# Performance work log

Measured on AMD Instinct MI355X. Metric: run time of the kernel, lower is better.

## Reference

```python
import jax, jax.numpy as jnp
import numpy as np

B, C, H, W = 4, 512, 64, 64
CQ = C // 8


def setup_inputs() -> dict:
    key = jax.random.key(0)
    ks = jax.random.split(key, 8)
    s_in = 1.0 / np.sqrt(C)
    return {
        "x": jax.random.normal(ks[0], (B, C, H, W), jnp.float32),
        "wq": jax.random.normal(ks[1], (CQ, C), jnp.float32) * s_in,
        "bq": jax.random.normal(ks[2], (CQ,), jnp.float32) * 0.01,
        "wk": jax.random.normal(ks[3], (CQ, C), jnp.float32) * s_in,
        "bk": jax.random.normal(ks[4], (CQ,), jnp.float32) * 0.01,
        "wv": jax.random.normal(ks[5], (C, C), jnp.float32) * s_in,
        "bv": jax.random.normal(ks[6], (C,), jnp.float32) * 0.01,
        "gamma": jax.random.normal(ks[7], (1,), jnp.float32) * 0.1,
    }


def reference(x, wq, bq, wk, bk, wv, bv, gamma):
    b, c, h, w = x.shape
    n = h * w
    xf = x.reshape(b, c, n)  # [B, C, N]; 1x1 conv == channel matmul
    q = jnp.einsum("oc,bcn->bon", wq, xf) + bq[None, :, None]  # [B, CQ, N]
    k = jnp.einsum("oc,bcn->bon", wk, xf) + bk[None, :, None]  # [B, CQ, N]
    v = jnp.einsum("oc,bcn->bon", wv, xf) + bv[None, :, None]  # [B, C, N]
    energy = jnp.einsum("bcn,bcm->bnm", q, k)  # [B, N, N]
    attn = jax.nn.softmax(energy, axis=-1)
    out = jnp.einsum("bcm,bnm->bcn", v, attn)  # [B, C, N]
    out = out.reshape(b, c, h, w)
    return gamma[0] * out + x
```

## Files before the change

kernel.cpp:

```cpp
#include <hip/hip_runtime.h>
#include <hip/hip_bf16.h>

#define BATCH 4
#define CH    512
#define NPIX  4096
#define LOG2E 1.4426950408889634f

#define BOFF  327680
#define WTOT  328320
#define PSTR 264

typedef float v4f __attribute__((ext_vector_type(4)));
typedef short v8s __attribute__((ext_vector_type(8)));
typedef unsigned short u16;

__device__ __forceinline__ float b2f(u16 v){
    union { unsigned u; float f; } x; x.u = ((unsigned)v) << 16; return x.f;
}
__device__ __forceinline__ u16 f2b(float f){
    union { float f; unsigned u; } x; x.f = f;
    unsigned r = x.u + 0x7fffu + ((x.u >> 16) & 1u);
    return (u16)(r >> 16);
}
__device__ __forceinline__ void f2b2(float a, float b, u16* o){
    union { __hip_bfloat162 v; u16 s[2]; } u;
    u.v = __float22bfloat162_rn(make_float2(a, b));
    o[0] = u.s[0]; o[1] = u.s[1];
}
__device__ __forceinline__ v4f mfma16(v8s a, v8s b, v4f c){
    return __builtin_amdgcn_mfma_f32_16x16x32_bf16(a, b, c, 0, 0, 0);
}
__device__ __forceinline__ float load_s(const void* p, size_t idx, int isf32){
    return isf32 ? ((const float*)p)[idx] : b2f(((const u16*)p)[idx]);
}

__global__ void detect_kernel(const unsigned* __restrict__ x, int* __restrict__ flag){
    __shared__ int cnt;
    if (threadIdx.x == 0) cnt = 0;
    __syncthreads();
    int c = 0;
    for (int i = threadIdx.x; i < 1024; i += 64){
        unsigned e = (x[i] >> 23) & 0xFFu;
        if (e >= 64u && e < 192u) c++;
    }
    atomicAdd(&cnt, c);
    __syncthreads();
    if (threadIdx.x == 0) flag[0] = (cnt > 512) ? 1 : 0;
}

__global__ __launch_bounds__(256) void prep_kernel(
    const void* __restrict__ wq, const void* __restrict__ bq,
    const void* __restrict__ wk, const void* __restrict__ bk,
    const void* __restrict__ wv, const void* __restrict__ bv,
    u16* __restrict__ wall, const int* __restrict__ flag)
{
    const int isf32 = flag[0];
    int i = blockIdx.x * 256 + threadIdx.x;
    if (i >= WTOT) return;
    float v;
    if (i < BOFF){
        int o = i >> 9, c = i & 511;
        if (o < 64)       v = load_s(wq, (size_t)o * 512 + c, isf32);
        else if (o < 128) v = load_s(wk, (size_t)(o - 64) * 512 + c, isf32);
        else              v = load_s(wv, (size_t)(o - 128) * 512 + c, isf32);
    } else {
        int o = i - BOFF;
        if (o < 64)       v = load_s(bq, o, isf32);
        else if (o < 128) v = load_s(bk, o - 64, isf32);
        else              v = load_s(bv, o - 128, isf32);
    }
    wall[i] = f2b(v);
}

__global__ __launch_bounds__(512, 2) void proj_kernel(
    const void* __restrict__ x, const u16* __restrict__ wall,
    u16* __restrict__ Qf, u16* __restrict__ Kf, u16* __restrict__ Vf,
    u16* __restrict__ xbf, const int* __restrict__ flag)
{
    const int isf32 = flag[0];
    const int ntile = blockIdx.x, b = blockIdx.y;
    const int n0 = ntile * 64;
    const int t = threadIdx.x, lane = t & 63, w = t >> 6, q = lane >> 4, col = lane & 15;

    __shared__ __align__(16) u16 xT[2][64 * 40];

    const int rrow  = t >> 4;
    const int ncol4 = (t & 15) * 4;
    const size_t xbase = (size_t)b * CH * NPIX + n0 + ncol4;

    v4f acc[5][4];
    #pragma unroll
    for (int i = 0; i < 5; i++)
        #pragma unroll
        for (int j = 0; j < 4; j++) acc[i][j] = (v4f){0.f, 0.f, 0.f, 0.f};

    #define LOADX(dst_f4, cb_) do {                                          \
        const size_t src = xbase + (size_t)((cb_) * 32 + rrow) * NPIX;       \
        if (isf32) dst_f4 = *(const float4*)((const float*)x + src);         \
        else {                                                               \
            union { uint2 v; float2 f; } ldu;                                \
            ldu.v = *(const uint2*)((const u16*)x + src);                    \
            dst_f4.x = ldu.f.x; dst_f4.y = ldu.f.y; dst_f4.z = 0; dst_f4.w = 0; \
        }                                                                    \
    } while (0)

    #define CVT4(vals_, f4_) do {                                            \
        if (isf32){ f2b2(f4_.x, f4_.y, &vals_[0]); f2b2(f4_.z, f4_.w, &vals_[2]); } \
        else { union { float2 f; uint2 v; } uu; uu.f = make_float2(f4_.x, f4_.y);   \
               union { uint2 v; u16 s[4]; } ss; ss.v = uu.v;                 \
               vals_[0]=ss.s[0]; vals_[1]=ss.s[1]; vals_[2]=ss.s[2]; vals_[3]=ss.s[3]; } \
    } while (0)

    float4 g_next;
    {
        float4 g0; LOADX(g0, 0);
        u16 vals[4]; CVT4(vals, g0);
        #pragma unroll
        for (int i = 0; i < 4; i++) xT[0][(ncol4 + i) * 40 + rrow] = vals[i];
        *(uint2*)&xbf[(size_t)(b * CH + rrow) * NPIX + n0 + ncol4] = *(uint2*)vals;
        LOADX(g_next, 1);
    }
    __syncthreads();

    for (int cb = 0; cb < 16; cb++){
        const int buf = cb & 1;
        const int c0 = cb * 32 + q * 8;

        v8s wf[5];
        #pragma unroll
        for (int ct = 0; ct < 5; ct++)
            wf[ct] = *(const v8s*)&wall[(size_t)(80 * w + 16 * ct + col) * 512 + c0];

        v8s a[4];
        #pragma unroll
        for (int g = 0; g < 4; g++)
            a[g] = *(const v8s*)&xT[buf][(16 * g + col) * 40 + q * 8];

        if (cb < 15){
            u16 vals[4]; CVT4(vals, g_next);
            #pragma unroll
            for (int i = 0; i < 4; i++) xT[buf ^ 1][(ncol4 + i) * 40 + rrow] = vals[i];
            *(uint2*)&xbf[(size_t)(b * CH + (cb + 1) * 32 + rrow) * NPIX + n0 + ncol4] = *(uint2*)vals;
            if (cb < 14) LOADX(g_next, cb + 2);
        }

        #pragma unroll
        for (int ct = 0; ct < 5; ct++)
            #pragma unroll
            for (int g = 0; g < 4; g++)
                acc[ct][g] = mfma16(a[g], wf[ct], acc[ct][g]);
        __syncthreads();
    }
    #undef LOADX
    #undef CVT4

    const u16* ball = wall + BOFF;
    #pragma unroll
    for (int ct = 0; ct < 5; ct++){
        const int o = 80 * w + 16 * ct + col;
        const float bv_ = b2f(ball[o]);
        #pragma unroll
        for (int g = 0; g < 4; g++){
            const int nb = n0 + 16 * g + 4 * q;
            if (o < 64){
                const int k = o;
                size_t base = (size_t)b * NPIX * 64
                    + ((size_t)((nb >> 4) * 2 + (k >> 5))) * 512
                    + ((k & 31) >> 3) * 128 + (nb & 15) * 8 + (k & 7);
                #pragma unroll
                for (int r = 0; r < 4; r++)
                    Qf[base + r * 8] = f2b((acc[ct][g][r] + bv_) * LOG2E);
            } else if (o < 128){
                const int k = o - 64;
                size_t base = (size_t)b * NPIX * 64
                    + ((size_t)((nb >> 4) * 2 + (k >> 5))) * 512
                    + ((k & 31) >> 3) * 128 + (nb & 15) * 8 + (k & 7);
                #pragma unroll
                for (int r = 0; r < 4; r++)
                    Kf[base + r * 8] = f2b(acc[ct][g][r] + bv_);
            } else {
                const int c = o - 128;
                size_t base = (size_t)b * CH * NPIX
                    + ((size_t)((c >> 4) * 128 + (nb >> 5))) * 512
                    + ((nb & 31) >> 3) * 128 + (c & 15) * 8 + (nb & 7);
                union { uint2 u; u16 s[4]; } ov;
                #pragma unroll
                for (int r = 0; r < 4; r++)
                    ov.s[r] = f2b(acc[ct][g][r] + bv_);
                *(uint2*)&Vf[base] = ov.u;
            }
        }
    }
}

__global__ __launch_bounds__(512, 2) void attn_kernel(
    const u16* __restrict__ Qf, const u16* __restrict__ Kf, const u16* __restrict__ Vf,
    const u16* __restrict__ xbf, const void* __restrict__ gamma,
    void* __restrict__ out, const int* __restrict__ flag)
{
    const int isf32 = flag[0];
    const int bid = blockIdx.x;
    const int csplit = bid & 1;
    const int b      = (bid >> 1) & 3;
    const int ntile  = bid >> 3;
    const int n0 = ntile * 128;

    const int t = threadIdx.x, lane = t & 63, w = t >> 6, q = lane >> 4, col = lane & 15;
    const int nh = w & 1;
    const int ws = w >> 1;

    __shared__ __align__(16) u16  Plds[2][128 * PSTR];
    __shared__ __align__(16) float lsum[8][64];

    const u16* Qb = Qf + (size_t)b * NPIX * 64;
    const u16* Kb = Kf + (size_t)b * NPIX * 64;
    const u16* Vb = Vf + (size_t)b * CH * NPIX;

    v8s qa[4][2];
    #pragma unroll
    for (int g = 0; g < 4; g++)
        #pragma unroll
        for (int c2 = 0; c2 < 2; c2++)
            qa[g][c2] = *(const v8s*)&Qb[(size_t)((((n0 + 64 * nh) >> 4) + g) * 2 + c2) * 512 + lane * 8];

    float lreg[4][4];
    #pragma unroll
    for (int g = 0; g < 4; g++)
        #pragma unroll
        for (int r = 0; r < 4; r++) lreg[g][r] = 0.f;

    v4f oacc[4][4];
    #pragma unroll
    for (int i = 0; i < 4; i++)
        #pragma unroll
        for (int j = 0; j < 4; j++) oacc[i][j] = (v4f){0.f, 0.f, 0.f, 0.f};

    const int ms    = 64 * ws;
    const int cslab = csplit * 256 + 64 * ws;

    for (int it = 0; it < 16; it++){
        const int m0 = it * 256;
        const int buf = it & 1;

        v8s kf[4][2];
        #pragma unroll
        for (int mt = 0; mt < 4; mt++)
            #pragma unroll
            for (int c2 = 0; c2 < 2; c2++)
                kf[mt][c2] = *(const v8s*)&Kb[(size_t)((((m0 + ms) >> 4) + mt) * 2 + c2) * 512 + lane * 8];

        #pragma unroll
        for (int g = 0; g < 4; g++){
            #pragma unroll
            for (int mt = 0; mt < 4; mt++){
                v4f sv = (v4f){-64.f, -64.f, -64.f, -64.f};
                sv = mfma16(qa[g][0], kf[mt][0], sv);
                sv = mfma16(qa[g][1], kf[mt][1], sv);
                #pragma unroll
                for (int r = 0; r < 4; r++){
                    float p = exp2f(fminf(sv[r], 30.f));
                    lreg[g][r] += p;
                    Plds[buf][(64 * nh + 16 * g + 4 * q + r) * PSTR + ms + 16 * mt + col] = f2b(p);
                }
            }
        }

        __syncthreads();

        v8s va_c[4];
        #pragma unroll
        for (int ct = 0; ct < 4; ct++)
            va_c[ct] = *(const v8s*)&Vb[(size_t)(((cslab + 16 * ct) >> 4) * 128 + (m0 >> 5)) * 512 + lane * 8];
        #pragma unroll
        for (int kk = 0; kk < 8; kk++){
            v8s va_n[4];
            if (kk < 7){
                #pragma unroll
                for (int ct = 0; ct < 4; ct++)
                    va_n[ct] = *(const v8s*)&Vb[(size_t)(((cslab + 16 * ct) >> 4) * 128 + (m0 >> 5) + kk + 1) * 512 + lane * 8];
            }
            v8s pb[4];
            #pragma unroll
            for (int nt = 0; nt < 4; nt++)
                pb[nt] = *(const v8s*)&Plds[buf][(64 * nh + 16 * nt + col) * PSTR + 32 * kk + q * 8];
            #pragma unroll
            for (int ct = 0; ct < 4; ct++)
                #pragma unroll
                for (int nt = 0; nt < 4; nt++)
                    oacc[ct][nt] = mfma16(va_c[ct], pb[nt], oacc[ct][nt]);
            #pragma unroll
            for (int ct = 0; ct < 4; ct++) va_c[ct] = va_n[ct];
        }
    }

    #pragma unroll
    for (int mk = 1; mk < 16; mk <<= 1)
        #pragma unroll
        for (int g = 0; g < 4; g++)
            #pragma unroll
            for (int r = 0; r < 4; r++)
                lreg[g][r] += __shfl_xor(lreg[g][r], mk);
    if (col == 0){
        #pragma unroll
        for (int g = 0; g < 4; g++)
            #pragma unroll
            for (int r = 0; r < 4; r++)
                lsum[w][16 * g + 4 * q + r] = lreg[g][r];
    }
    __syncthreads();

    const float gam = load_s(gamma, 0, isf32);
    float linv[4];
    #pragma unroll
    for (int nt = 0; nt < 4; nt++){
        int nn = 16 * nt + col;
        float l = lsum[nh][nn] + lsum[2 + nh][nn] + lsum[4 + nh][nn] + lsum[6 + nh][nn];
        linv[nt] = gam / l;
    }

    const size_t boff = (size_t)b * CH * NPIX;
    #pragma unroll
    for (int ct = 0; ct < 4; ct++){
        #pragma unroll
        for (int rr = 0; rr < 4; rr++){
            int c = cslab + 16 * ct + 4 * q + rr;
            size_t base = boff + (size_t)c * NPIX + n0 + 64 * nh;
            #pragma unroll
            for (int nt = 0; nt < 4; nt++){
                int n = 16 * nt + col;
                float o = oacc[ct][nt][rr] * linv[nt] + b2f(xbf[base + n]);
                if (isf32) ((float*)out)[base + n] = o;
                else       ((u16*)out)[base + n]  = f2b(o);
            }
        }
    }
}

extern "C" void kernel_launch(void* const* d_in, const int* in_sizes, int n_in,
                              void* d_out, int out_size, void* d_ws, size_t ws_size,
                              hipStream_t stream)
{
    const void* x     = d_in[0];
    const void* wq    = d_in[1];
    const void* bq    = d_in[2];
    const void* wk    = d_in[3];
    const void* bk    = d_in[4];
    const void* wv    = d_in[5];
    const void* bv    = d_in[6];
    const void* gamma = d_in[7];

    u16* Qf   = (u16*)d_ws;
    u16* Kf   = Qf + (size_t)1048576;
    u16* Vf   = Kf + (size_t)1048576;
    u16* xbf  = Vf + (size_t)8388608;
    u16* wall = xbf + (size_t)8388608;
    int* flag = (int*)(wall + WTOT + 16);

    detect_kernel<<<1, 64, 0, stream>>>((const unsigned*)x, flag);
    prep_kernel<<<(WTOT + 255) / 256, 256, 0, stream>>>(wq, bq, wk, bk, wv, bv, wall, flag);
    proj_kernel<<<dim3(64, BATCH), 512, 0, stream>>>(x, wall, Qf, Kf, Vf, xbf, flag);
    attn_kernel<<<256, 512, 0, stream>>>(Qf, Kf, Vf, xbf, gamma, d_out, flag);
}
```

Before: 234.7 us.

## Transpose score MFMA, pack P stores, prefetch K and double-buffer V loads

Swaps the MFMA operand order so each lane holds four consecutive key columns of one query row. This lets the softmax probabilities be packed into a single 8-byte LDS store, and the row sums need fewer shuffles. It also prefetches the next K tile into a double-buffered register set, loads V two steps ahead, uses the raw hardware exp2 builtin without clamping, and pads the LDS row stride. These changes target LDS store count, shuffle overhead and global load latency, at the cost of more registers and no overflow clamp on the exponent.

```diff
diff --git a/kernel.cpp b/kernel.cpp
--- a/kernel.cpp
+++ b/kernel.cpp
@@ -8,7 +8,7 @@
 
 #define BOFF  327680
 #define WTOT  328320
-#define PSTR 264
+#define PSTR  268
 
 typedef float v4f __attribute__((ext_vector_type(4)));
 typedef short v8s __attribute__((ext_vector_type(8)));
@@ -26,6 +26,13 @@
     union { __hip_bfloat162 v; u16 s[2]; } u;
     u.v = __float22bfloat162_rn(make_float2(a, b));
     o[0] = u.s[0]; o[1] = u.s[1];
+}
+__device__ __forceinline__ float fexp2(float x){
+#if __has_builtin(__builtin_amdgcn_exp2f)
+    return __builtin_amdgcn_exp2f(x);
+#else
+    return exp2f(x);
+#endif
 }
 __device__ __forceinline__ v4f mfma16(v8s a, v8s b, v4f c){
     return __builtin_amdgcn_mfma_f32_16x16x32_bf16(a, b, c, 0, 0, 0);
@@ -223,11 +230,7 @@
         for (int c2 = 0; c2 < 2; c2++)
             qa[g][c2] = *(const v8s*)&Qb[(size_t)((((n0 + 64 * nh) >> 4) + g) * 2 + c2) * 512 + lane * 8];
 
-    float lreg[4][4];
-    #pragma unroll
-    for (int g = 0; g < 4; g++)
-        #pragma unroll
-        for (int r = 0; r < 4; r++) lreg[g][r] = 0.f;
+    float lreg[4] = {0.f, 0.f, 0.f, 0.f};
 
     v4f oacc[4][4];
     #pragma unroll
@@ -238,47 +241,55 @@
     const int ms    = 64 * ws;
     const int cslab = csplit * 256 + 64 * ws;
 
+    v8s kfb[2][4][2];
+    #pragma unroll
+    for (int mt = 0; mt < 4; mt++)
+        #pragma unroll
+        for (int c2 = 0; c2 < 2; c2++)
+            kfb[0][mt][c2] = *(const v8s*)&Kb[(size_t)(((ms >> 4) + mt) * 2 + c2) * 512 + lane * 8];
+
+    #pragma unroll 2
     for (int it = 0; it < 16; it++){
         const int m0 = it * 256;
         const int buf = it & 1;
 
-        v8s kf[4][2];
-        #pragma unroll
-        for (int mt = 0; mt < 4; mt++)
-            #pragma unroll
-            for (int c2 = 0; c2 < 2; c2++)
-                kf[mt][c2] = *(const v8s*)&Kb[(size_t)((((m0 + ms) >> 4) + mt) * 2 + c2) * 512 + lane * 8];
-
         #pragma unroll
         for (int g = 0; g < 4; g++){
             #pragma unroll
             for (int mt = 0; mt < 4; mt++){
                 v4f sv = (v4f){-64.f, -64.f, -64.f, -64.f};
-                sv = mfma16(qa[g][0], kf[mt][0], sv);
-                sv = mfma16(qa[g][1], kf[mt][1], sv);
-                #pragma unroll
-                for (int r = 0; r < 4; r++){
-                    float p = exp2f(fminf(sv[r], 30.f));
-                    lreg[g][r] += p;
-                    Plds[buf][(64 * nh + 16 * g + 4 * q + r) * PSTR + ms + 16 * mt + col] = f2b(p);
-                }
+                sv = mfma16(kfb[buf][mt][0], qa[g][0], sv);
+                sv = mfma16(kfb[buf][mt][1], qa[g][1], sv);
+                float p0 = fexp2(sv[0]), p1 = fexp2(sv[1]);
+                float p2 = fexp2(sv[2]), p3 = fexp2(sv[3]);
+                lreg[g] += (p0 + p1) + (p2 + p3);
+                union { uint2 u; u16 s[4]; } pk;
+                f2b2(p0, p1, &pk.s[0]);
+                f2b2(p2, p3, &pk.s[2]);
+                *(uint2*)&Plds[buf][(64 * nh + 16 * g + col) * PSTR + ms + 16 * mt + 4 * q] = pk.u;
             }
         }
 
         __syncthreads();
 
-        v8s va_c[4];
-        #pragma unroll
-        for (int ct = 0; ct < 4; ct++)
-            va_c[ct] = *(const v8s*)&Vb[(size_t)(((cslab + 16 * ct) >> 4) * 128 + (m0 >> 5)) * 512 + lane * 8];
+        if (it < 15){
+            const int m1 = (it + 1) * 256;
+            #pragma unroll
+            for (int mt = 0; mt < 4; mt++)
+                #pragma unroll
+                for (int c2 = 0; c2 < 2; c2++)
+                    kfb[buf ^ 1][mt][c2] = *(const v8s*)&Kb[(size_t)((((m1 + ms) >> 4) + mt) * 2 + c2) * 512 + lane * 8];
+        }
+
+        v8s vab[2][4];
+        #pragma unroll
+        for (int ct = 0; ct < 4; ct++){
+            vab[0][ct] = *(const v8s*)&Vb[(size_t)(((cslab + 16 * ct) >> 4) * 128 + (m0 >> 5) + 0) * 512 + lane * 8];
+            vab[1][ct] = *(const v8s*)&Vb[(size_t)(((cslab + 16 * ct) >> 4) * 128 + (m0 >> 5) + 1) * 512 + lane * 8];
+        }
         #pragma unroll
         for (int kk = 0; kk < 8; kk++){
-            v8s va_n[4];
-            if (kk < 7){
-                #pragma unroll
-                for (int ct = 0; ct < 4; ct++)
-                    va_n[ct] = *(const v8s*)&Vb[(size_t)(((cslab + 16 * ct) >> 4) * 128 + (m0 >> 5) + kk + 1) * 512 + lane * 8];
-            }
+            const int cur = kk & 1;
             v8s pb[4];
             #pragma unroll
             for (int nt = 0; nt < 4; nt++)
@@ -287,25 +298,24 @@
             for (int ct = 0; ct < 4; ct++)
                 #pragma unroll
                 for (int nt = 0; nt < 4; nt++)
-                    oacc[ct][nt] = mfma16(va_c[ct], pb[nt], oacc[ct][nt]);
-            #pragma unroll
-            for (int ct = 0; ct < 4; ct++) va_c[ct] = va_n[ct];
-        }
-    }
-
-    #pragma unroll
-    for (int mk = 1; mk < 16; mk <<= 1)
+                    oacc[ct][nt] = mfma16(vab[cur][ct], pb[nt], oacc[ct][nt]);
+            if (kk < 6){
+                #pragma unroll
+                for (int ct = 0; ct < 4; ct++)
+                    vab[cur][ct] = *(const v8s*)&Vb[(size_t)(((cslab + 16 * ct) >> 4) * 128 + (m0 >> 5) + kk + 2) * 512 + lane * 8];
+            }
+        }
+    }
+
+    #pragma unroll
+    for (int g = 0; g < 4; g++){
+        lreg[g] += __shfl_xor(lreg[g], 16);
+        lreg[g] += __shfl_xor(lreg[g], 32);
+    }
+    if (lane < 16){
         #pragma unroll
         for (int g = 0; g < 4; g++)
-            #pragma unroll
-            for (int r = 0; r < 4; r++)
-                lreg[g][r] += __shfl_xor(lreg[g][r], mk);
-    if (col == 0){
-        #pragma unroll
-        for (int g = 0; g < 4; g++)
-            #pragma unroll
-            for (int r = 0; r < 4; r++)
-                lsum[w][16 * g + 4 * q + r] = lreg[g][r];
+            lsum[w][16 * g + lane] = lreg[g];
     }
     __syncthreads();
 
```

Measured after the change: 311.8 us. 1.33x slower.
